# Optimization experiments

Measured on AMD Instinct MI355X. Metric: run time of the kernel, lower is better.

Reference implementation:

```python
import jax, jax.numpy as jnp
import numpy as np

B, T, HID = 2, 2048, 2048
NH, NKV, HD = 16, 4, 128
GROUPS = NH // NKV

def _rotate_half(t):
    t1, t2 = jnp.split(t, 2, axis=-1)
    return jnp.concatenate([-t2, t1], axis=-1)

def _apply_rotary(t, cos, sin):
    # t: [B, H, T, D], cos/sin: [1, 1, T, D]
    return t * cos + _rotate_half(t) * sin

def setup_inputs() -> dict:
    key = jax.random.key(0)
    ks = jax.random.split(key, 6)
    x = jax.random.normal(ks[0], (B, T, HID), dtype=jnp.float32)
    # real rotary tables
    inv_freq = 1.0 / (10000.0 ** (jnp.arange(0, HD, 2, dtype=jnp.float32) / HD))
    pos = jnp.arange(T, dtype=jnp.float32)
    freqs = jnp.outer(pos, inv_freq)            # [T, D/2]
    emb = jnp.concatenate([freqs, freqs], -1)   # [T, D]
    cos = jnp.cos(emb)[None, None]              # [1,1,T,D]
    sin = jnp.sin(emb)[None, None]
    s = 0.02
    Wq = jax.random.normal(ks[1], (HID, NH * HD), dtype=jnp.float32) * s
    Wk = jax.random.normal(ks[2], (HID, NKV * HD), dtype=jnp.float32) * s
    Wv = jax.random.normal(ks[3], (HID, NKV * HD), dtype=jnp.float32) * s
    Wo = jax.random.normal(ks[4], (NH * HD, HID), dtype=jnp.float32) * s
    return {"x": x, "cos": cos, "sin": sin, "Wq": Wq, "Wk": Wk, "Wv": Wv, "Wo": Wo}

def reference(x, cos, sin, Wq, Wk, Wv, Wo):
    b, t, _ = x.shape
    q = (x @ Wq).reshape(b, t, NH, HD).transpose(0, 2, 1, 3)    # [B,NH,T,D]
    k = (x @ Wk).reshape(b, t, NKV, HD).transpose(0, 2, 1, 3)   # [B,NKV,T,D]
    v = (x @ Wv).reshape(b, t, NKV, HD).transpose(0, 2, 1, 3)
    q = _apply_rotary(q, cos, sin)
    k = _apply_rotary(k, cos, sin)
    # GQA without repeat_interleave: group q-heads by kv-head
    qg = q.reshape(b, NKV, GROUPS, t, HD)                       # [B,KV,G,T,D]
    scale = 1.0 / jnp.sqrt(jnp.float32(HD))
    scores = jnp.einsum('bkgtd,bksd->bkgts', qg, k) * scale     # [B,KV,G,T,S]
    causal = jnp.tril(jnp.ones((t, t), dtype=bool))
    scores = jnp.where(causal[None, None, None], scores, jnp.float32(-1e30))
    attn = jax.nn.softmax(scores, axis=-1)
    out = jnp.einsum('bkgts,bksd->bkgtd', attn, v)              # [B,KV,G,T,D]
    out = out.reshape(b, NH, t, HD).transpose(0, 2, 1, 3).reshape(b, t, NH * HD)
    return out @ Wo
```

## Files before the change

kernel.cpp:

```cpp
#include <hip/hip_runtime.h>
#include <hip/hip_bf16.h>
#include <cstdint>

typedef unsigned short u16;
typedef unsigned int u32;
typedef __bf16 bf16x8 __attribute__((ext_vector_type(8)));
typedef float f32x4 __attribute__((ext_vector_type(4)));

#define BDIM 2
#define TDIM 2048
#define HIDDIM 2048
#define NHEAD 16
#define NKVH 4
#define HD 128
#define MROWS (BDIM*TDIM)
#define NQKV 3072
#define KDIM 2048

#define MFMA16(a,b,c) __builtin_amdgcn_mfma_f32_16x16x32_bf16((a),(b),(c),0,0,0)

__device__ __forceinline__ u16 f2bf(float f) {
    __bf16 h = (__bf16)f;
    return __builtin_bit_cast(u16, h);
}
__device__ __forceinline__ float bf2f(u32 u) {
    u <<= 16;
    return __builtin_bit_cast(float, u);
}
__device__ __forceinline__ void gld16(const void* g, void* l) {
    __builtin_amdgcn_global_load_lds(
        (const __attribute__((address_space(1))) u32*)g,
        (__attribute__((address_space(3))) u32*)l, 16, 0, 0);
}

__global__ __launch_bounds__(256) void cvt_x_kernel(const float* __restrict__ x,
                                                    u16* __restrict__ o) {
    size_t i = ((size_t)blockIdx.x * 256 + threadIdx.x) * 8;
    float4 a = *(const float4*)(x + i);
    float4 b = *(const float4*)(x + i + 4);
    uint4 v;
    v.x = (u32)f2bf(a.x) | ((u32)f2bf(a.y) << 16);
    v.y = (u32)f2bf(a.z) | ((u32)f2bf(a.w) << 16);
    v.z = (u32)f2bf(b.x) | ((u32)f2bf(b.y) << 16);
    v.w = (u32)f2bf(b.z) | ((u32)f2bf(b.w) << 16);
    *(uint4*)(o + i) = v;
}

__global__ __launch_bounds__(256) void transpose_cvt(const float* __restrict__ src,
                                                     u16* __restrict__ dst, int N) {
    __shared__ float tile[32][33];
    int tx = threadIdx.x, ty = threadIdx.y;
    int n0 = blockIdx.x * 32, k0 = blockIdx.y * 32;
#pragma unroll
    for (int r = 0; r < 4; r++)
        tile[ty + 8*r][tx] = src[(size_t)(k0 + ty + 8*r) * N + n0 + tx];
    __syncthreads();
#pragma unroll
    for (int r = 0; r < 4; r++)
        dst[(size_t)(n0 + ty + 8*r) * KDIM + k0 + tx] = f2bf(tile[tx][ty + 8*r]);
}

template<int OUT_BF16>
__global__ void __launch_bounds__(256, 2) gemm_bt(const u16* __restrict__ A,
                                                  const u16* __restrict__ Bt,
                                                  void* __restrict__ C, int ldc) {
    __shared__ __align__(16) u16 Al[128 * 32];
    __shared__ __align__(16) u16 Bl[128 * 32];
    const int tid = threadIdx.x;
    const int lane = tid & 63;
    const int w = tid >> 6;
    const int wm = (w & 1) * 64;
    const int wn = (w >> 1) * 64;
    const int quad = lane >> 4;
    const int l15 = lane & 15;
    const size_t bm = (size_t)blockIdx.x * 128;
    const size_t bn = (size_t)blockIdx.y * 128;

    const int srow = lane >> 2;
    const int kq = (lane & 3) ^ ((lane >> 3) & 3);
    const int i0 = 2 * w, i1 = 2 * w + 1;

    const u16* ga0 = A + (bm + i0*16 + srow) * KDIM + kq * 8;
    const u16* ga1 = A + (bm + i1*16 + srow) * KDIM + kq * 8;
    const u16* gb0 = Bt + (bn + i0*16 + srow) * KDIM + kq * 8;
    const u16* gb1 = Bt + (bn + i1*16 + srow) * KDIM + kq * 8;

    const int swz = ((quad ^ ((l15 >> 1) & 3)) << 3);
    int aoff[4], boff[4];
#pragma unroll
    for (int t = 0; t < 4; t++) {
        aoff[t] = (wm + t*16 + l15) * 32 + swz;
        boff[t] = (wn + t*16 + l15) * 32 + swz;
    }

    f32x4 acc[4][4] = {};

    for (int kt = 0; kt < KDIM / 32; kt++) {
        gld16(ga0 + kt*32, &Al[i0 * 512]);
        gld16(ga1 + kt*32, &Al[i1 * 512]);
        gld16(gb0 + kt*32, &Bl[i0 * 512]);
        gld16(gb1 + kt*32, &Bl[i1 * 512]);
        __syncthreads();
        bf16x8 af[4], bfv[4];
#pragma unroll
        for (int t = 0; t < 4; t++) {
            af[t]  = *(const bf16x8*)&Al[aoff[t]];
            bfv[t] = *(const bf16x8*)&Bl[boff[t]];
        }
#pragma unroll
        for (int mt = 0; mt < 4; mt++)
#pragma unroll
            for (int nt = 0; nt < 4; nt++)
                acc[mt][nt] = MFMA16(af[mt], bfv[nt], acc[mt][nt]);
        __syncthreads();
    }

#pragma unroll
    for (int mt = 0; mt < 4; mt++) {
        size_t m0 = bm + wm + mt*16 + quad*4;
#pragma unroll
        for (int nt = 0; nt < 4; nt++) {
            size_t n = bn + wn + nt*16 + l15;
#pragma unroll
            for (int r = 0; r < 4; r++) {
                if (OUT_BF16)
                    ((u16*)C)[(m0 + r) * (size_t)ldc + n] = f2bf(acc[mt][nt][r]);
                else
                    ((float*)C)[(m0 + r) * (size_t)ldc + n] = acc[mt][nt][r];
            }
        }
    }
}

__global__ __launch_bounds__(256) void rotary_kernel(u16* __restrict__ QKV,
                                                     const float* __restrict__ cosT,
                                                     const float* __restrict__ sinT) {
    int i = blockIdx.x * 256 + threadIdx.x;
    int m = i / 320;
    int rem = i - m * 320;
    int head = rem >> 4;
    int d0 = (rem & 15) << 2;
    int t = m & (TDIM - 1);
    int col;
    float sc;
    if (head < NHEAD) {
        col = head * HD + d0;
        sc = 0.08838834764831845f * 1.4426950408889634f;
    } else {
        col = HIDDIM + (head - NHEAD) * HD + d0;
        sc = 1.0f;
    }
    u16* p0 = QKV + (size_t)m * NQKV + col;
    u16* p1 = p0 + 64;
    float4 cv = *(const float4*)(cosT + t * HD + d0);
    float4 sv = *(const float4*)(sinT + t * HD + d0);
    uint2 qa = *(const uint2*)p0;
    uint2 qb = *(const uint2*)p1;
    float f0[4] = { bf2f(qa.x & 0xffffu), bf2f(qa.x >> 16), bf2f(qa.y & 0xffffu), bf2f(qa.y >> 16) };
    float f1[4] = { bf2f(qb.x & 0xffffu), bf2f(qb.x >> 16), bf2f(qb.y & 0xffffu), bf2f(qb.y >> 16) };
    float c[4] = { cv.x, cv.y, cv.z, cv.w };
    float s[4] = { sv.x, sv.y, sv.z, sv.w };
    u16 o0[4], o1[4];
#pragma unroll
    for (int k = 0; k < 4; k++) {
        o0[k] = f2bf((f0[k] * c[k] - f1[k] * s[k]) * sc);
        o1[k] = f2bf((f1[k] * c[k] + f0[k] * s[k]) * sc);
    }
    uint2 w0, w1;
    w0.x = (u32)o0[0] | ((u32)o0[1] << 16);
    w0.y = (u32)o0[2] | ((u32)o0[3] << 16);
    w1.x = (u32)o1[0] | ((u32)o1[1] << 16);
    w1.y = (u32)o1[2] | ((u32)o1[3] << 16);
    *(uint2*)p0 = w0;
    *(uint2*)p1 = w1;
}

__global__ void __launch_bounds__(256, 2) attn_kernel(const u16* __restrict__ QKV,
                                                      u16* __restrict__ AO) {
    constexpr int LK = 152;
    constexpr int LP = 72;
    constexpr int LV = 72;
    __shared__ __align__(16) u16 Kl[64 * LK];
    __shared__ __align__(16) u16 Vt[128 * LV];

    const int qt = blockIdx.x;
    const int h  = blockIdx.y;
    const int b  = blockIdx.z;
    const int kh = h >> 2;
    const int tid = threadIdx.x;
    const int lane = tid & 63;
    const int w = tid >> 6;
    const int quad = lane >> 4;
    const int l15 = lane & 15;

    const size_t rowbase = (size_t)b * TDIM;
    const u16* Qb = QKV + (rowbase + qt * 128) * NQKV + h * HD;
    const u16* Kb = QKV + rowbase * NQKV + HIDDIM + kh * HD;
    const u16* Vb = QKV + rowbase * NQKV + HIDDIM + NKVH * HD + kh * HD;

    bf16x8 qf[2][4];
#pragma unroll
    for (int mt = 0; mt < 2; mt++) {
        const u16* qr = Qb + (size_t)(w*32 + mt*16 + l15) * NQKV;
#pragma unroll
        for (int kt = 0; kt < 4; kt++)
            qf[mt][kt] = *(const bf16x8*)(qr + kt*32 + quad*8);
    }

    f32x4 O[2][8] = {};
    float mrun[2][4], lrun[2][4];
#pragma unroll
    for (int mt = 0; mt < 2; mt++)
#pragma unroll
        for (int r = 0; r < 4; r++) { mrun[mt][r] = -1e30f; lrun[mt][r] = 0.0f; }

    const int jmax = 2 * qt + 1;
    for (int j = 0; j <= jmax; j++) {
#pragma unroll
        for (int i = 0; i < 4; i++) {
            int c = tid + 256 * i;
            int s = c >> 4, ch = c & 15;
            uint4 v = *(const uint4*)(Kb + (size_t)(j*64 + s) * NQKV + ch*8);
            *(uint4*)&Kl[s * LK + ch * 8] = v;
        }
#pragma unroll
        for (int i = 0; i < 2; i++) {
            int u = tid + 256 * i;
            int sp = u & 31, dch = u >> 5;
            int s = sp * 2, d0 = dch * 8;
            const u16* g0 = Vb + (size_t)(j*64 + s) * NQKV + d0;
            uint4 r0 = *(const uint4*)g0;
            uint4 r1 = *(const uint4*)(g0 + NQKV);
            u32 ra[4] = { r0.x, r0.y, r0.z, r0.w };
            u32 rb[4] = { r1.x, r1.y, r1.z, r1.w };
#pragma unroll
            for (int k2 = 0; k2 < 4; k2++) {
                u32 lo = (ra[k2] & 0xffffu) | (rb[k2] << 16);
                u32 hi = (ra[k2] >> 16) | (rb[k2] & 0xffff0000u);
                *(u32*)&Vt[(d0 + 2*k2)     * LV + s] = lo;
                *(u32*)&Vt[(d0 + 2*k2 + 1) * LV + s] = hi;
            }
        }
        __syncthreads();

        f32x4 S[2][4] = {};
#pragma unroll
        for (int kt = 0; kt < 4; kt++) {
#pragma unroll
            for (int nt = 0; nt < 4; nt++) {
                bf16x8 bfr = *(const bf16x8*)&Kl[(nt*16 + l15) * LK + kt*32 + quad*8];
                S[0][nt] = MFMA16(qf[0][kt], bfr, S[0][nt]);
                S[1][nt] = MFMA16(qf[1][kt], bfr, S[1][nt]);
            }
        }

        if (j >= 2 * qt) {
            int sbase = j * 64;
            int tbase = qt * 128 + w * 32;
#pragma unroll
            for (int mt = 0; mt < 2; mt++)
#pragma unroll
                for (int nt = 0; nt < 4; nt++) {
                    int scol = sbase + nt*16 + l15;
#pragma unroll
                    for (int r = 0; r < 4; r++) {
                        int trow = tbase + mt*16 + quad*4 + r;
                        if (scol > trow) S[mt][nt][r] = -1e30f;
                    }
                }
        }

        float alpha[2][4];
#pragma unroll
        for (int mt = 0; mt < 2; mt++) {
#pragma unroll
            for (int r = 0; r < 4; r++) {
                float mx = S[mt][0][r];
                mx = fmaxf(mx, S[mt][1][r]);
                mx = fmaxf(mx, S[mt][2][r]);
                mx = fmaxf(mx, S[mt][3][r]);
                mx = fmaxf(mx, __shfl_xor(mx, 1));
                mx = fmaxf(mx, __shfl_xor(mx, 2));
                mx = fmaxf(mx, __shfl_xor(mx, 4));
                mx = fmaxf(mx, __shfl_xor(mx, 8));
                float mnew = fmaxf(mrun[mt][r], mx);
                float al = __builtin_amdgcn_exp2f(mrun[mt][r] - mnew);
                mrun[mt][r] = mnew;
                alpha[mt][r] = al;
                float rs = 0.0f;
#pragma unroll
                for (int nt = 0; nt < 4; nt++) {
                    float p = __builtin_amdgcn_exp2f(S[mt][nt][r] - mnew);
                    S[mt][nt][r] = p;
                    rs += p;
                }
                rs += __shfl_xor(rs, 1);
                rs += __shfl_xor(rs, 2);
                rs += __shfl_xor(rs, 4);
                rs += __shfl_xor(rs, 8);
                lrun[mt][r] = lrun[mt][r] * al + rs;
            }
        }
#pragma unroll
        for (int mt = 0; mt < 2; mt++)
#pragma unroll
            for (int nt = 0; nt < 8; nt++)
#pragma unroll
                for (int r = 0; r < 4; r++)
                    O[mt][nt][r] *= alpha[mt][r];

        __syncthreads();
#pragma unroll
        for (int mt = 0; mt < 2; mt++)
#pragma unroll
            for (int nt = 0; nt < 4; nt++)
#pragma unroll
                for (int r = 0; r < 4; r++)
                    Kl[(w*32 + mt*16 + quad*4 + r) * LP + nt*16 + l15] = f2bf(S[mt][nt][r]);
        __syncthreads();

#pragma unroll
        for (int kt = 0; kt < 2; kt++) {
            bf16x8 pa[2];
#pragma unroll
            for (int mt = 0; mt < 2; mt++)
                pa[mt] = *(const bf16x8*)&Kl[(w*32 + mt*16 + l15) * LP + kt*32 + quad*8];
#pragma unroll
            for (int nt = 0; nt < 8; nt++) {
                bf16x8 bv = *(const bf16x8*)&Vt[(nt*16 + l15) * LV + kt*32 + quad*8];
                O[0][nt] = MFMA16(pa[0], bv, O[0][nt]);
                O[1][nt] = MFMA16(pa[1], bv, O[1][nt]);
            }
        }
        __syncthreads();
    }

#pragma unroll
    for (int mt = 0; mt < 2; mt++) {
        float inv[4];
#pragma unroll
        for (int r = 0; r < 4; r++) inv[r] = 1.0f / lrun[mt][r];
        size_t row0 = rowbase + qt*128 + w*32 + mt*16 + quad*4;
#pragma unroll
        for (int nt = 0; nt < 8; nt++) {
            size_t cix = (size_t)h * HD + nt*16 + l15;
#pragma unroll
            for (int r = 0; r < 4; r++)
                AO[(row0 + r) * HIDDIM + cix] = f2bf(O[mt][nt][r] * inv[r]);
        }
    }
}

extern "C" void kernel_launch(void* const* d_in, const int* in_sizes, int n_in,
                              void* d_out, int out_size, void* d_ws, size_t ws_size,
                              hipStream_t stream) {
    (void)in_sizes; (void)n_in; (void)out_size; (void)ws_size;
    const float* x    = (const float*)d_in[0];
    const float* cosT = (const float*)d_in[1];
    const float* sinT = (const float*)d_in[2];
    const float* Wq   = (const float*)d_in[3];
    const float* Wk   = (const float*)d_in[4];
    const float* Wv   = (const float*)d_in[5];
    const float* Wo   = (const float*)d_in[6];

    char* ws = (char*)d_ws;
    u16* QKV   = (u16*)ws;
    u16* xb    = (u16*)(ws + (size_t)MROWS * NQKV * 2);
    u16* Wqkvt = (u16*)(ws + (size_t)MROWS * NQKV * 2 + (size_t)MROWS * HIDDIM * 2);
    u16* Wot   = Wqkvt + (size_t)NQKV * KDIM;

    cvt_x_kernel<<<4096, 256, 0, stream>>>(x, xb);
    dim3 tb(32, 8);
    transpose_cvt<<<dim3(64, 64), tb, 0, stream>>>(Wq, Wqkvt, 2048);
    transpose_cvt<<<dim3(16, 64), tb, 0, stream>>>(Wk, Wqkvt + (size_t)2048 * KDIM, 512);
    transpose_cvt<<<dim3(16, 64), tb, 0, stream>>>(Wv, Wqkvt + (size_t)2560 * KDIM, 512);
    transpose_cvt<<<dim3(64, 64), tb, 0, stream>>>(Wo, Wot, 2048);

    gemm_bt<1><<<dim3(32, 24), 256, 0, stream>>>(xb, Wqkvt, QKV, NQKV);
    rotary_kernel<<<5120, 256, 0, stream>>>(QKV, cosT, sinT);
    attn_kernel<<<dim3(16, 16, 2), 256, 0, stream>>>(QKV, xb);
    gemm_bt<0><<<dim3(32, 16), 256, 0, stream>>>(xb, Wot, d_out, HIDDIM);
}
```

Before: 373.3 us.

## Pair causal query tiles per block and swizzle K tile in LDS

Each attention block now processes two 64-row query tiles, qt and 31-qt, in sequence. This evens out the causal work across blocks, which previously varied with the 128-row tile index. K tiles are loaded with a direct global-to-LDS copy into an unpadded, XOR-swizzled layout, replacing the padded register round-trip. Each wave now handles 16 query rows instead of 32, so K/V data is reused less per LDS load, but register pressure drops.

```diff
diff --git a/kernel.cpp b/kernel.cpp
--- a/kernel.cpp
+++ b/kernel.cpp
@@ -177,13 +177,12 @@
 
 __global__ void __launch_bounds__(256, 2) attn_kernel(const u16* __restrict__ QKV,
                                                       u16* __restrict__ AO) {
-    constexpr int LK = 152;
+    constexpr int LV = 72;
     constexpr int LP = 72;
-    constexpr int LV = 72;
-    __shared__ __align__(16) u16 Kl[64 * LK];
+    __shared__ __align__(16) u16 Kl[64 * 128];
     __shared__ __align__(16) u16 Vt[128 * LV];
 
-    const int qt = blockIdx.x;
+    const int pa = blockIdx.x;
     const int h  = blockIdx.y;
     const int b  = blockIdx.z;
     const int kh = h >> 2;
@@ -194,159 +193,143 @@
     const int l15 = lane & 15;
 
     const size_t rowbase = (size_t)b * TDIM;
-    const u16* Qb = QKV + (rowbase + qt * 128) * NQKV + h * HD;
+    const u16* Qb = QKV + rowbase * NQKV + h * HD;
     const u16* Kb = QKV + rowbase * NQKV + HIDDIM + kh * HD;
-    const u16* Vb = QKV + rowbase * NQKV + HIDDIM + NKVH * HD + kh * HD;
-
-    bf16x8 qf[2][4];
-#pragma unroll
-    for (int mt = 0; mt < 2; mt++) {
-        const u16* qr = Qb + (size_t)(w*32 + mt*16 + l15) * NQKV;
-#pragma unroll
-        for (int kt = 0; kt < 4; kt++)
-            qf[mt][kt] = *(const bf16x8*)(qr + kt*32 + quad*8);
-    }
-
-    f32x4 O[2][8] = {};
-    float mrun[2][4], lrun[2][4];
-#pragma unroll
-    for (int mt = 0; mt < 2; mt++)
-#pragma unroll
-        for (int r = 0; r < 4; r++) { mrun[mt][r] = -1e30f; lrun[mt][r] = 0.0f; }
-
-    const int jmax = 2 * qt + 1;
-    for (int j = 0; j <= jmax; j++) {
-#pragma unroll
-        for (int i = 0; i < 4; i++) {
-            int c = tid + 256 * i;
-            int s = c >> 4, ch = c & 15;
-            uint4 v = *(const uint4*)(Kb + (size_t)(j*64 + s) * NQKV + ch*8);
-            *(uint4*)&Kl[s * LK + ch * 8] = v;
-        }
-#pragma unroll
-        for (int i = 0; i < 2; i++) {
-            int u = tid + 256 * i;
-            int sp = u & 31, dch = u >> 5;
-            int s = sp * 2, d0 = dch * 8;
-            const u16* g0 = Vb + (size_t)(j*64 + s) * NQKV + d0;
-            uint4 r0 = *(const uint4*)g0;
-            uint4 r1 = *(const uint4*)(g0 + NQKV);
-            u32 ra[4] = { r0.x, r0.y, r0.z, r0.w };
-            u32 rb[4] = { r1.x, r1.y, r1.z, r1.w };
-#pragma unroll
-            for (int k2 = 0; k2 < 4; k2++) {
-                u32 lo = (ra[k2] & 0xffffu) | (rb[k2] << 16);
-                u32 hi = (ra[k2] >> 16) | (rb[k2] & 0xffff0000u);
-                *(u32*)&Vt[(d0 + 2*k2)     * LV + s] = lo;
-                *(u32*)&Vt[(d0 + 2*k2 + 1) * LV + s] = hi;
-            }
-        }
-        __syncthreads();
-
-        f32x4 S[2][4] = {};
-#pragma unroll
-        for (int kt = 0; kt < 4; kt++) {
-#pragma unroll
-            for (int nt = 0; nt < 4; nt++) {
-                bf16x8 bfr = *(const bf16x8*)&Kl[(nt*16 + l15) * LK + kt*32 + quad*8];
-                S[0][nt] = MFMA16(qf[0][kt], bfr, S[0][nt]);
-                S[1][nt] = MFMA16(qf[1][kt], bfr, S[1][nt]);
-            }
-        }
-
-        if (j >= 2 * qt) {
-            int sbase = j * 64;
-            int tbase = qt * 128 + w * 32;
-#pragma unroll
-            for (int mt = 0; mt < 2; mt++)
+    const u16* Vb = Kb + NKVH * HD;
+
+    int krow[4], kgch[4];
+#pragma unroll
+    for (int i = 0; i < 4; i++) {
+        krow[i] = w*16 + i*4 + quad;
+        kgch[i] = l15 ^ (krow[i] & 7);
+    }
+
+#pragma unroll 1
+    for (int ph = 0; ph < 2; ph++) {
+        const int qt = ph ? (31 - pa) : pa;
+
+        bf16x8 qf[4];
+        {
+            const u16* qr = Qb + (size_t)(qt*64 + w*16 + l15) * NQKV;
+#pragma unroll
+            for (int kt = 0; kt < 4; kt++)
+                qf[kt] = *(const bf16x8*)(qr + kt*32 + quad*8);
+        }
+        f32x4 O[8] = {};
+        float mrun[4], lrun[4];
+#pragma unroll
+        for (int r = 0; r < 4; r++) { mrun[r] = -1e30f; lrun[r] = 0.0f; }
+
+#pragma unroll 1
+        for (int j = 0; j <= qt; j++) {
+#pragma unroll
+            for (int i = 0; i < 4; i++) {
+                const u16* g = Kb + (size_t)(j*64 + krow[i]) * NQKV + kgch[i]*8;
+                gld16(g, &Kl[(w*16 + i*4) * 128]);
+            }
+#pragma unroll
+            for (int i = 0; i < 2; i++) {
+                int u = tid + 256*i;
+                int sp = u & 31, dch = u >> 5;
+                int s = sp*2, d0 = dch*8;
+                const u16* g0 = Vb + (size_t)(j*64 + s) * NQKV + d0;
+                uint4 r0 = *(const uint4*)g0;
+                uint4 r1 = *(const uint4*)(g0 + NQKV);
+                u32 ra[4] = { r0.x, r0.y, r0.z, r0.w };
+                u32 rb[4] = { r1.x, r1.y, r1.z, r1.w };
+#pragma unroll
+                for (int k2 = 0; k2 < 4; k2++) {
+                    u32 lo = (ra[k2] & 0xffffu) | (rb[k2] << 16);
+                    u32 hi = (ra[k2] >> 16) | (rb[k2] & 0xffff0000u);
+                    *(u32*)&Vt[(d0 + 2*k2)     * LV + s] = lo;
+                    *(u32*)&Vt[(d0 + 2*k2 + 1) * LV + s] = hi;
+                }
+            }
+            __syncthreads();
+
+            f32x4 S[4] = {};
+#pragma unroll
+            for (int kt = 0; kt < 4; kt++) {
+                int p = (kt*4 + quad) ^ (l15 & 7);
 #pragma unroll
                 for (int nt = 0; nt < 4; nt++) {
-                    int scol = sbase + nt*16 + l15;
-#pragma unroll
-                    for (int r = 0; r < 4; r++) {
-                        int trow = tbase + mt*16 + quad*4 + r;
-                        if (scol > trow) S[mt][nt][r] = -1e30f;
-                    }
-                }
-        }
-
-        float alpha[2][4];
-#pragma unroll
-        for (int mt = 0; mt < 2; mt++) {
+                    bf16x8 bfr = *(const bf16x8*)&Kl[(nt*16 + l15)*128 + p*8];
+                    S[nt] = MFMA16(qf[kt], bfr, S[nt]);
+                }
+            }
+
+            if (j == qt) {
+                int toff = w*16 + quad*4;
+#pragma unroll
+                for (int nt = 0; nt < 4; nt++) {
+                    int scol = nt*16 + l15;
+#pragma unroll
+                    for (int r = 0; r < 4; r++)
+                        if (scol > toff + r) S[nt][r] = -1e30f;
+                }
+            }
+
+            float alpha[4];
 #pragma unroll
             for (int r = 0; r < 4; r++) {
-                float mx = S[mt][0][r];
-                mx = fmaxf(mx, S[mt][1][r]);
-                mx = fmaxf(mx, S[mt][2][r]);
-                mx = fmaxf(mx, S[mt][3][r]);
+                float mx = fmaxf(fmaxf(S[0][r], S[1][r]), fmaxf(S[2][r], S[3][r]));
                 mx = fmaxf(mx, __shfl_xor(mx, 1));
                 mx = fmaxf(mx, __shfl_xor(mx, 2));
                 mx = fmaxf(mx, __shfl_xor(mx, 4));
                 mx = fmaxf(mx, __shfl_xor(mx, 8));
-                float mnew = fmaxf(mrun[mt][r], mx);
-                float al = __builtin_amdgcn_exp2f(mrun[mt][r] - mnew);
-                mrun[mt][r] = mnew;
-                alpha[mt][r] = al;
+                float mnew = fmaxf(mrun[r], mx);
+                float al = __builtin_amdgcn_exp2f(mrun[r] - mnew);
+                mrun[r] = mnew;
+                alpha[r] = al;
                 float rs = 0.0f;
 #pragma unroll
                 for (int nt = 0; nt < 4; nt++) {
-                    float p = __builtin_amdgcn_exp2f(S[mt][nt][r] - mnew);
-                    S[mt][nt][r] = p;
+                    float p = __builtin_amdgcn_exp2f(S[nt][r] - mnew);
+                    S[nt][r] = p;
                     rs += p;
                 }
                 rs += __shfl_xor(rs, 1);
                 rs += __shfl_xor(rs, 2);
                 rs += __shfl_xor(rs, 4);
                 rs += __shfl_xor(rs, 8);
-                lrun[mt][r] = lrun[mt][r] * al + rs;
-            }
-        }
-#pragma unroll
-        for (int mt = 0; mt < 2; mt++)
+                lrun[r] = lrun[r] * al + rs;
+            }
 #pragma unroll
             for (int nt = 0; nt < 8; nt++)
 #pragma unroll
                 for (int r = 0; r < 4; r++)
-                    O[mt][nt][r] *= alpha[mt][r];
-
-        __syncthreads();
-#pragma unroll
-        for (int mt = 0; mt < 2; mt++)
+                    O[nt][r] *= alpha[r];
+
+            __syncthreads();
 #pragma unroll
             for (int nt = 0; nt < 4; nt++)
 #pragma unroll
                 for (int r = 0; r < 4; r++)
-                    Kl[(w*32 + mt*16 + quad*4 + r) * LP + nt*16 + l15] = f2bf(S[mt][nt][r]);
-        __syncthreads();
-
-#pragma unroll
-        for (int kt = 0; kt < 2; kt++) {
-            bf16x8 pa[2];
-#pragma unroll
-            for (int mt = 0; mt < 2; mt++)
-                pa[mt] = *(const bf16x8*)&Kl[(w*32 + mt*16 + l15) * LP + kt*32 + quad*8];
-#pragma unroll
-            for (int nt = 0; nt < 8; nt++) {
-                bf16x8 bv = *(const bf16x8*)&Vt[(nt*16 + l15) * LV + kt*32 + quad*8];
-                O[0][nt] = MFMA16(pa[0], bv, O[0][nt]);
-                O[1][nt] = MFMA16(pa[1], bv, O[1][nt]);
-            }
-        }
-        __syncthreads();
-    }
-
-#pragma unroll
-    for (int mt = 0; mt < 2; mt++) {
+                    Kl[(w*16 + quad*4 + r) * LP + nt*16 + l15] = f2bf(S[nt][r]);
+            __syncthreads();
+
+#pragma unroll
+            for (int kt = 0; kt < 2; kt++) {
+                bf16x8 pa_f = *(const bf16x8*)&Kl[(w*16 + l15) * LP + kt*32 + quad*8];
+#pragma unroll
+                for (int nt = 0; nt < 8; nt++) {
+                    bf16x8 bv = *(const bf16x8*)&Vt[(nt*16 + l15) * LV + kt*32 + quad*8];
+                    O[nt] = MFMA16(pa_f, bv, O[nt]);
+                }
+            }
+            __syncthreads();
+        }
+
         float inv[4];
 #pragma unroll
-        for (int r = 0; r < 4; r++) inv[r] = 1.0f / lrun[mt][r];
-        size_t row0 = rowbase + qt*128 + w*32 + mt*16 + quad*4;
+        for (int r = 0; r < 4; r++) inv[r] = 1.0f / lrun[r];
+        size_t row0 = rowbase + qt*64 + w*16 + quad*4;
 #pragma unroll
         for (int nt = 0; nt < 8; nt++) {
             size_t cix = (size_t)h * HD + nt*16 + l15;
 #pragma unroll
             for (int r = 0; r < 4; r++)
-                AO[(row0 + r) * HIDDIM + cix] = f2bf(O[mt][nt][r] * inv[r]);
+                AO[(row0 + r) * HIDDIM + cix] = f2bf(O[nt][r] * inv[r]);
         }
     }
 }
```

Measured after the change: 334.8 us. 10.3% less time.

## Balance causal attention tiles and prefetch K/V into registers

Applied to the files above, without the earlier changes.

Each attention block now processes two query tiles (qt and 15-qt), which evens out the causal workload and halves the grid. The next K/V tile is prefetched into registers while the current one is computed. P gets its own LDS buffer, which removes one barrier per iteration. K is stored with an XOR swizzle instead of padding. Warps whose rows are fully masked skip compute, row reductions use DPP instead of shuffles, and O rescaling is skipped when no max changed. The risks are higher register pressure and only 256 blocks, which may underfill the device.

```diff
diff --git a/kernel.cpp b/kernel.cpp
--- a/kernel.cpp
+++ b/kernel.cpp
@@ -31,6 +31,27 @@
     __builtin_amdgcn_global_load_lds(
         (const __attribute__((address_space(1))) u32*)g,
         (__attribute__((address_space(3))) u32*)l, 16, 0, 0);
+}
+
+template<int CTRL>
+__device__ __forceinline__ float dpp_rot(float x) {
+    return __builtin_bit_cast(float,
+        __builtin_amdgcn_update_dpp(0, __builtin_bit_cast(int, x),
+                                    CTRL, 0xf, 0xf, true));
+}
+__device__ __forceinline__ float rowmax16(float x) {
+    x = fmaxf(x, dpp_rot<0x121>(x));
+    x = fmaxf(x, dpp_rot<0x122>(x));
+    x = fmaxf(x, dpp_rot<0x124>(x));
+    x = fmaxf(x, dpp_rot<0x128>(x));
+    return x;
+}
+__device__ __forceinline__ float rowsum16(float x) {
+    x += dpp_rot<0x121>(x);
+    x += dpp_rot<0x122>(x);
+    x += dpp_rot<0x124>(x);
+    x += dpp_rot<0x128>(x);
+    return x;
 }
 
 __global__ __launch_bounds__(256) void cvt_x_kernel(const float* __restrict__ x,
@@ -177,13 +198,13 @@
 
 __global__ void __launch_bounds__(256, 2) attn_kernel(const u16* __restrict__ QKV,
                                                       u16* __restrict__ AO) {
-    constexpr int LK = 152;
+    constexpr int LV = 72;
     constexpr int LP = 72;
-    constexpr int LV = 72;
-    __shared__ __align__(16) u16 Kl[64 * LK];
+    __shared__ __align__(16) u16 Kl[64 * 128];
     __shared__ __align__(16) u16 Vt[128 * LV];
-
-    const int qt = blockIdx.x;
+    __shared__ __align__(16) u16 Pl[128 * LP];
+
+    const int pa = blockIdx.x;
     const int h  = blockIdx.y;
     const int b  = blockIdx.z;
     const int kh = h >> 2;
@@ -194,159 +215,196 @@
     const int l15 = lane & 15;
 
     const size_t rowbase = (size_t)b * TDIM;
-    const u16* Qb = QKV + (rowbase + qt * 128) * NQKV + h * HD;
+    const u16* Qb = QKV + rowbase * NQKV + h * HD;
     const u16* Kb = QKV + rowbase * NQKV + HIDDIM + kh * HD;
-    const u16* Vb = QKV + rowbase * NQKV + HIDDIM + NKVH * HD + kh * HD;
-
-    bf16x8 qf[2][4];
-#pragma unroll
-    for (int mt = 0; mt < 2; mt++) {
-        const u16* qr = Qb + (size_t)(w*32 + mt*16 + l15) * NQKV;
-#pragma unroll
-        for (int kt = 0; kt < 4; kt++)
-            qf[mt][kt] = *(const bf16x8*)(qr + kt*32 + quad*8);
-    }
-
-    f32x4 O[2][8] = {};
-    float mrun[2][4], lrun[2][4];
-#pragma unroll
-    for (int mt = 0; mt < 2; mt++)
-#pragma unroll
-        for (int r = 0; r < 4; r++) { mrun[mt][r] = -1e30f; lrun[mt][r] = 0.0f; }
-
-    const int jmax = 2 * qt + 1;
-    for (int j = 0; j <= jmax; j++) {
-#pragma unroll
-        for (int i = 0; i < 4; i++) {
-            int c = tid + 256 * i;
-            int s = c >> 4, ch = c & 15;
-            uint4 v = *(const uint4*)(Kb + (size_t)(j*64 + s) * NQKV + ch*8);
-            *(uint4*)&Kl[s * LK + ch * 8] = v;
-        }
-#pragma unroll
-        for (int i = 0; i < 2; i++) {
-            int u = tid + 256 * i;
-            int sp = u & 31, dch = u >> 5;
-            int s = sp * 2, d0 = dch * 8;
-            const u16* g0 = Vb + (size_t)(j*64 + s) * NQKV + d0;
-            uint4 r0 = *(const uint4*)g0;
-            uint4 r1 = *(const uint4*)(g0 + NQKV);
-            u32 ra[4] = { r0.x, r0.y, r0.z, r0.w };
-            u32 rb[4] = { r1.x, r1.y, r1.z, r1.w };
-#pragma unroll
-            for (int k2 = 0; k2 < 4; k2++) {
-                u32 lo = (ra[k2] & 0xffffu) | (rb[k2] << 16);
-                u32 hi = (ra[k2] >> 16) | (rb[k2] & 0xffff0000u);
-                *(u32*)&Vt[(d0 + 2*k2)     * LV + s] = lo;
-                *(u32*)&Vt[(d0 + 2*k2 + 1) * LV + s] = hi;
+    const u16* Vb = Kb + NKVH * HD;
+
+    const int kch = tid & 15;
+    int kprow[4];
+#pragma unroll
+    for (int i = 0; i < 4; i++) kprow[i] = (tid >> 4) + 16*i;
+    const int sp0 = tid & 31, dch0 = tid >> 5, dch1 = dch0 + 8;
+
+#pragma unroll 1
+    for (int ph = 0; ph < 2; ph++) {
+        const int qt = ph ? (15 - pa) : pa;
+        const int jend = 2*qt + 1;
+
+        bf16x8 qf[2][4];
+#pragma unroll
+        for (int mt = 0; mt < 2; mt++) {
+            const u16* qr = Qb + (size_t)(qt*128 + w*32 + mt*16 + l15) * NQKV;
+#pragma unroll
+            for (int kt = 0; kt < 4; kt++)
+                qf[mt][kt] = *(const bf16x8*)(qr + kt*32 + quad*8);
+        }
+        f32x4 O[2][8] = {};
+        float mrun[2][4], lrun[2][4];
+#pragma unroll
+        for (int mt = 0; mt < 2; mt++)
+#pragma unroll
+            for (int r = 0; r < 4; r++) { mrun[mt][r] = -1e30f; lrun[mt][r] = 0.0f; }
+
+        uint4 kr[4];
+#pragma unroll
+        for (int i = 0; i < 4; i++)
+            kr[i] = *(const uint4*)(Kb + (size_t)kprow[i] * NQKV + kch*8);
+        uint4 vr0a, vr0b, vr1a, vr1b;
+        {
+            const u16* g0 = Vb + (size_t)(sp0*2) * NQKV + dch0*8;
+            vr0a = *(const uint4*)g0;
+            vr0b = *(const uint4*)(g0 + NQKV);
+            const u16* g1 = Vb + (size_t)(sp0*2) * NQKV + dch1*8;
+            vr1a = *(const uint4*)g1;
+            vr1b = *(const uint4*)(g1 + NQKV);
+        }
+
+#pragma unroll 1
+        for (int j = 0; j <= jend; j++) {
+#pragma unroll
+            for (int i = 0; i < 4; i++)
+                *(uint4*)&Kl[kprow[i]*128 + (kch ^ (kprow[i] & 7))*8] = kr[i];
+            {
+                u32 ra[4] = { vr0a.x, vr0a.y, vr0a.z, vr0a.w };
+                u32 rb[4] = { vr0b.x, vr0b.y, vr0b.z, vr0b.w };
+                int s = sp0*2, d0 = dch0*8;
+#pragma unroll
+                for (int k2 = 0; k2 < 4; k2++) {
+                    u32 lo = (ra[k2] & 0xffffu) | (rb[k2] << 16);
+                    u32 hi = (ra[k2] >> 16) | (rb[k2] & 0xffff0000u);
+                    *(u32*)&Vt[(d0 + 2*k2)     * LV + s] = lo;
+                    *(u32*)&Vt[(d0 + 2*k2 + 1) * LV + s] = hi;
+                }
+                u32 rc[4] = { vr1a.x, vr1a.y, vr1a.z, vr1a.w };
+                u32 rd[4] = { vr1b.x, vr1b.y, vr1b.z, vr1b.w };
+                d0 = dch1*8;
+#pragma unroll
+                for (int k2 = 0; k2 < 4; k2++) {
+                    u32 lo = (rc[k2] & 0xffffu) | (rd[k2] << 16);
+                    u32 hi = (rc[k2] >> 16) | (rd[k2] & 0xffff0000u);
+                    *(u32*)&Vt[(d0 + 2*k2)     * LV + s] = lo;
+                    *(u32*)&Vt[(d0 + 2*k2 + 1) * LV + s] = hi;
+                }
             }
-        }
-        __syncthreads();
-
-        f32x4 S[2][4] = {};
-#pragma unroll
-        for (int kt = 0; kt < 4; kt++) {
-#pragma unroll
-            for (int nt = 0; nt < 4; nt++) {
-                bf16x8 bfr = *(const bf16x8*)&Kl[(nt*16 + l15) * LK + kt*32 + quad*8];
-                S[0][nt] = MFMA16(qf[0][kt], bfr, S[0][nt]);
-                S[1][nt] = MFMA16(qf[1][kt], bfr, S[1][nt]);
+            __syncthreads();
+
+            if (j < jend) {
+                const u16* Kbn = Kb + (size_t)(j+1) * 64 * NQKV;
+#pragma unroll
+                for (int i = 0; i < 4; i++)
+                    kr[i] = *(const uint4*)(Kbn + (size_t)kprow[i] * NQKV + kch*8);
+                const u16* Vbn = Vb + (size_t)(j+1) * 64 * NQKV;
+                const u16* g0 = Vbn + (size_t)(sp0*2) * NQKV + dch0*8;
+                vr0a = *(const uint4*)g0;
+                vr0b = *(const uint4*)(g0 + NQKV);
+                const u16* g1 = Vbn + (size_t)(sp0*2) * NQKV + dch1*8;
+                vr1a = *(const uint4*)g1;
+                vr1b = *(const uint4*)(g1 + NQKV);
             }
-        }
-
-        if (j >= 2 * qt) {
-            int sbase = j * 64;
-            int tbase = qt * 128 + w * 32;
-#pragma unroll
-            for (int mt = 0; mt < 2; mt++)
-#pragma unroll
-                for (int nt = 0; nt < 4; nt++) {
-                    int scol = sbase + nt*16 + l15;
+
+            if (j*64 <= qt*128 + w*32 + 31) {
+                f32x4 S[2][4] = {};
+#pragma unroll
+                for (int kt = 0; kt < 4; kt++) {
+                    int p = (kt*4 + quad) ^ (l15 & 7);
+#pragma unroll
+                    for (int nt = 0; nt < 4; nt++) {
+                        bf16x8 bfr = *(const bf16x8*)&Kl[(nt*16 + l15)*128 + p*8];
+                        S[0][nt] = MFMA16(qf[0][kt], bfr, S[0][nt]);
+                        S[1][nt] = MFMA16(qf[1][kt], bfr, S[1][nt]);
+                    }
+                }
+
+                if (j >= 2*qt) {
+                    int tbase = qt*128 + w*32;
+                    int sbase = j*64;
+#pragma unroll
+                    for (int mt = 0; mt < 2; mt++)
+#pragma unroll
+                        for (int nt = 0; nt < 4; nt++) {
+                            int scol = sbase + nt*16 + l15;
+#pragma unroll
+                            for (int r = 0; r < 4; r++) {
+                                int trow = tbase + mt*16 + quad*4 + r;
+                                if (scol > trow) S[mt][nt][r] = -1e30f;
+                            }
+                        }
+                }
+
+                float alpha[2][4];
+#pragma unroll
+                for (int mt = 0; mt < 2; mt++)
 #pragma unroll
                     for (int r = 0; r < 4; r++) {
-                        int trow = tbase + mt*16 + quad*4 + r;
-                        if (scol > trow) S[mt][nt][r] = -1e30f;
+                        float mx = fmaxf(fmaxf(S[mt][0][r], S[mt][1][r]),
+                                         fmaxf(S[mt][2][r], S[mt][3][r]));
+                        mx = rowmax16(mx);
+                        float mnew = fmaxf(mrun[mt][r], mx);
+                        float al = __builtin_amdgcn_exp2f(mrun[mt][r] - mnew);
+                        mrun[mt][r] = mnew;
+                        alpha[mt][r] = al;
+                        float rs = 0.0f;
+#pragma unroll
+                        for (int nt = 0; nt < 4; nt++) {
+                            float p = __builtin_amdgcn_exp2f(S[mt][nt][r] - mnew);
+                            S[mt][nt][r] = p;
+                            rs += p;
+                        }
+                        rs = rowsum16(rs);
+                        lrun[mt][r] = lrun[mt][r] * al + rs;
                     }
-                }
-        }
-
-        float alpha[2][4];
+                bool need = false;
+#pragma unroll
+                for (int mt = 0; mt < 2; mt++)
+#pragma unroll
+                    for (int r = 0; r < 4; r++) need |= (alpha[mt][r] < 1.0f);
+                if (__any(need)) {
+#pragma unroll
+                    for (int mt = 0; mt < 2; mt++)
+#pragma unroll
+                        for (int nt = 0; nt < 8; nt++)
+#pragma unroll
+                            for (int r = 0; r < 4; r++)
+                                O[mt][nt][r] *= alpha[mt][r];
+                }
+
+#pragma unroll
+                for (int mt = 0; mt < 2; mt++)
+#pragma unroll
+                    for (int nt = 0; nt < 4; nt++)
+#pragma unroll
+                        for (int r = 0; r < 4; r++)
+                            Pl[(w*32 + mt*16 + quad*4 + r) * LP + nt*16 + l15] =
+                                f2bf(S[mt][nt][r]);
+
+#pragma unroll
+                for (int kt = 0; kt < 2; kt++) {
+                    bf16x8 pa0 = *(const bf16x8*)&Pl[(w*32 + l15) * LP + kt*32 + quad*8];
+                    bf16x8 pa1 = *(const bf16x8*)&Pl[(w*32 + 16 + l15) * LP + kt*32 + quad*8];
+#pragma unroll
+                    for (int nt = 0; nt < 8; nt++) {
+                        bf16x8 bv = *(const bf16x8*)&Vt[(nt*16 + l15) * LV + kt*32 + quad*8];
+                        O[0][nt] = MFMA16(pa0, bv, O[0][nt]);
+                        O[1][nt] = MFMA16(pa1, bv, O[1][nt]);
+                    }
+                }
+            }
+            __syncthreads();
+        }
+
 #pragma unroll
         for (int mt = 0; mt < 2; mt++) {
-#pragma unroll
-            for (int r = 0; r < 4; r++) {
-                float mx = S[mt][0][r];
-                mx = fmaxf(mx, S[mt][1][r]);
-                mx = fmaxf(mx, S[mt][2][r]);
-                mx = fmaxf(mx, S[mt][3][r]);
-                mx = fmaxf(mx, __shfl_xor(mx, 1));
-                mx = fmaxf(mx, __shfl_xor(mx, 2));
-                mx = fmaxf(mx, __shfl_xor(mx, 4));
-                mx = fmaxf(mx, __shfl_xor(mx, 8));
-                float mnew = fmaxf(mrun[mt][r], mx);
-                float al = __builtin_amdgcn_exp2f(mrun[mt][r] - mnew);
-                mrun[mt][r] = mnew;
-                alpha[mt][r] = al;
-                float rs = 0.0f;
-#pragma unroll
-                for (int nt = 0; nt < 4; nt++) {
-                    float p = __builtin_amdgcn_exp2f(S[mt][nt][r] - mnew);
-                    S[mt][nt][r] = p;
-                    rs += p;
-                }
-                rs += __shfl_xor(rs, 1);
-                rs += __shfl_xor(rs, 2);
-                rs += __shfl_xor(rs, 4);
-                rs += __shfl_xor(rs, 8);
-                lrun[mt][r] = lrun[mt][r] * al + rs;
+            float inv[4];
+#pragma unroll
+            for (int r = 0; r < 4; r++) inv[r] = 1.0f / lrun[mt][r];
+            size_t row0 = rowbase + qt*128 + w*32 + mt*16 + quad*4;
+#pragma unroll
+            for (int nt = 0; nt < 8; nt++) {
+                size_t cix = (size_t)h * HD + nt*16 + l15;
+#pragma unroll
+                for (int r = 0; r < 4; r++)
+                    AO[(row0 + r) * HIDDIM + cix] = f2bf(O[mt][nt][r] * inv[r]);
             }
-        }
-#pragma unroll
-        for (int mt = 0; mt < 2; mt++)
-#pragma unroll
-            for (int nt = 0; nt < 8; nt++)
-#pragma unroll
-                for (int r = 0; r < 4; r++)
-                    O[mt][nt][r] *= alpha[mt][r];
-
-        __syncthreads();
-#pragma unroll
-        for (int mt = 0; mt < 2; mt++)
-#pragma unroll
-            for (int nt = 0; nt < 4; nt++)
-#pragma unroll
-                for (int r = 0; r < 4; r++)
-                    Kl[(w*32 + mt*16 + quad*4 + r) * LP + nt*16 + l15] = f2bf(S[mt][nt][r]);
-        __syncthreads();
-
-#pragma unroll
-        for (int kt = 0; kt < 2; kt++) {
-            bf16x8 pa[2];
-#pragma unroll
-            for (int mt = 0; mt < 2; mt++)
-                pa[mt] = *(const bf16x8*)&Kl[(w*32 + mt*16 + l15) * LP + kt*32 + quad*8];
-#pragma unroll
-            for (int nt = 0; nt < 8; nt++) {
-                bf16x8 bv = *(const bf16x8*)&Vt[(nt*16 + l15) * LV + kt*32 + quad*8];
-                O[0][nt] = MFMA16(pa[0], bv, O[0][nt]);
-                O[1][nt] = MFMA16(pa[1], bv, O[1][nt]);
-            }
-        }
-        __syncthreads();
-    }
-
-#pragma unroll
-    for (int mt = 0; mt < 2; mt++) {
-        float inv[4];
-#pragma unroll
-        for (int r = 0; r < 4; r++) inv[r] = 1.0f / lrun[mt][r];
-        size_t row0 = rowbase + qt*128 + w*32 + mt*16 + quad*4;
-#pragma unroll
-        for (int nt = 0; nt < 8; nt++) {
-            size_t cix = (size_t)h * HD + nt*16 + l15;
-#pragma unroll
-            for (int r = 0; r < 4; r++)
-                AO[(row0 + r) * HIDDIM + cix] = f2bf(O[mt][nt][r] * inv[r]);
         }
     }
 }
@@ -378,6 +436,6 @@
 
     gemm_bt<1><<<dim3(32, 24), 256, 0, stream>>>(xb, Wqkvt, QKV, NQKV);
     rotary_kernel<<<5120, 256, 0, stream>>>(QKV, cosT, sinT);
-    attn_kernel<<<dim3(16, 16, 2), 256, 0, stream>>>(QKV, xb);
+    attn_kernel<<<dim3(8, 16, 2), 256, 0, stream>>>(QKV, xb);
     gemm_bt<0><<<dim3(32, 16), 256, 0, stream>>>(xb, Wot, d_out, HIDDIM);
 }
```

Measured after the change: 353.2 us. 5.4% less time.
